# Optimization experiments

Hardware: AMD Instinct MI355X
Metric: run time of the kernel (lower is better)

## Reference

```python
import jax, jax.numpy as jnp
import numpy as np

N_NODES = 50000
N_EDGES = 800000
IN_FEATS = 512
NUM_HEADS = 4
OUT_FEATS = 64
NEG_SLOPE = 0.2


def setup_inputs() -> dict:
    key = jax.random.key(0)
    k1, k2, k3, k4, k5, k6 = jax.random.split(key, 6)
    feat = jax.random.normal(k1, (N_NODES, IN_FEATS), dtype=jnp.float32)
    W = jax.random.normal(k2, (IN_FEATS, NUM_HEADS * OUT_FEATS), dtype=jnp.float32) * (1.0 / np.sqrt(IN_FEATS))
    attn_l = jax.random.normal(k3, (NUM_HEADS, OUT_FEATS), dtype=jnp.float32) * (1.0 / np.sqrt(OUT_FEATS))
    attn_r = jax.random.normal(k4, (NUM_HEADS, OUT_FEATS), dtype=jnp.float32) * (1.0 / np.sqrt(OUT_FEATS))
    src = jax.random.randint(k5, (N_EDGES,), 0, N_NODES, dtype=jnp.int32)
    dst = jax.random.randint(k6, (N_EDGES,), 0, N_NODES, dtype=jnp.int32)
    return {"feat": feat, "W": W, "attn_l": attn_l, "attn_r": attn_r, "src": src, "dst": dst}


def reference(feat, W, attn_l, attn_r, src, dst):
    N = feat.shape[0]
    H, D = attn_l.shape
    # node-wise projection: fc(feat).view(N, H, D)
    ft = (feat @ W).reshape(N, H, D)
    # per-node attention logits
    el = jnp.einsum('nhd,hd->nh', ft, attn_l)  # [N, H]
    er = jnp.einsum('nhd,hd->nh', ft, attn_r)  # [N, H]
    # edge-wise score: leaky_relu(el[u] + er[v])
    e = jax.nn.leaky_relu(el[src] + er[dst], negative_slope=NEG_SLOPE)  # [E, H]
    # segment softmax over incoming edges of each destination node
    e_max = jax.ops.segment_max(e, dst, num_segments=N)  # [N, H]
    e_max = jnp.where(jnp.isfinite(e_max), e_max, 0.0)
    exp_e = jnp.exp(e - e_max[dst])  # [E, H]
    denom = jax.ops.segment_sum(exp_e, dst, num_segments=N)  # [N, H]
    a = exp_e / denom[dst]  # [E, H]
    # weighted message aggregation: sum_u a(u,v) * ft[u]
    msg = ft[src] * a[:, :, None]  # [E, H, D]
    out = jax.ops.segment_sum(msg, dst, num_segments=N)  # [N, H, D]
    return out.reshape(N, H * D)
```

## Files before the change

kernel.cpp:

```cpp
#include <hip/hip_runtime.h>
#include <hip/hip_fp16.h>

#define N_NODES 50000
#define N_EDGES 800000
#define IN_F    512
#define NH      4
#define DH      64
#define HD      256
#define NEG     0.2f
#define MAXDEG  64

typedef __attribute__((ext_vector_type(8))) short bf16x8;
typedef __attribute__((ext_vector_type(4))) float f32x4;

__device__ __forceinline__ unsigned short f2bf(float x) {
    unsigned u = __float_as_uint(x);
    unsigned r = (u + 0x7FFFu + ((u >> 16) & 1u)) >> 16;
    return (unsigned short)r;
}
__device__ __forceinline__ float bf2f(unsigned short b) {
    return __uint_as_float((unsigned)b << 16);
}
__device__ __forceinline__ unsigned short f2h(float x) {
    __half h = __float2half_rn(x);
    return *(unsigned short*)&h;
}
__device__ __forceinline__ float h2f(unsigned short us) {
    __half h = *(__half*)&us;
    return __half2float(h);
}

#define NZB ((N_NODES + 255) / 256)
__global__ __launch_bounds__(256) void setup_kernel(const float* __restrict__ W,
                                                    unsigned short* __restrict__ WtbT,
                                                    int* __restrict__ counts) {
    int b = blockIdx.x;
    if (b < NZB) {
        int i = b * 256 + threadIdx.x;
        if (i < N_NODES) counts[i] = 0;
    } else {
        int i = (b - NZB) * 256 + threadIdx.x;
        if (i < IN_F * HD) {
            int k = i >> 8;
            int n = i & 255;
            int t  = k >> 6;
            int kk = k & 63;
            int g  = kk >> 3;
            int w8 = kk & 7;
            WtbT[(size_t)t * 16384 + g * 2048 + n * 8 + w8] = f2bf(W[i]);
        }
    }
}

#define LDPA 72
__global__ __launch_bounds__(256) void gemm_kernel(const float* __restrict__ A,
                                                   const unsigned short* __restrict__ WtbT,
                                                   const float* __restrict__ attn_l,
                                                   const float* __restrict__ attn_r,
                                                   unsigned short* __restrict__ Cb,
                                                   float* __restrict__ el,
                                                   float* __restrict__ er) {
    __shared__ short A_s[2][64][LDPA];

    const int tid  = threadIdx.x;
    const int lane = tid & 63;
    const int w    = tid >> 6;
    const int lm   = lane & 15;
    const int quad = lane >> 4;
    const int row0 = blockIdx.x * 64;

    const int srow = tid >> 3;
    const int sc8  = (tid & 7) * 8;

    f32x4 acc[4][4] = {};
    float4 pa[4];

#define LOAD_A(KT)                                                             \
    {                                                                          \
        int g0 = row0 + srow; g0 = (g0 < N_NODES) ? g0 : (N_NODES - 1);        \
        const float* ap0 = A + (size_t)g0 * IN_F + (KT) + sc8;                 \
        pa[0] = *(const float4*)ap0; pa[1] = *(const float4*)(ap0 + 4);        \
        int g1 = row0 + 32 + srow; g1 = (g1 < N_NODES) ? g1 : (N_NODES - 1);   \
        const float* ap1 = A + (size_t)g1 * IN_F + (KT) + sc8;                 \
        pa[2] = *(const float4*)ap1; pa[3] = *(const float4*)(ap1 + 4);        \
    }

#define CVT_STORE(BUF)                                                         \
    {                                                                          \
        bf16x8 s;                                                              \
        s[0] = (short)f2bf(pa[0].x); s[1] = (short)f2bf(pa[0].y);              \
        s[2] = (short)f2bf(pa[0].z); s[3] = (short)f2bf(pa[0].w);              \
        s[4] = (short)f2bf(pa[1].x); s[5] = (short)f2bf(pa[1].y);              \
        s[6] = (short)f2bf(pa[1].z); s[7] = (short)f2bf(pa[1].w);              \
        *(bf16x8*)(&A_s[BUF][srow][sc8]) = s;                                  \
        s[0] = (short)f2bf(pa[2].x); s[1] = (short)f2bf(pa[2].y);              \
        s[2] = (short)f2bf(pa[2].z); s[3] = (short)f2bf(pa[2].w);              \
        s[4] = (short)f2bf(pa[3].x); s[5] = (short)f2bf(pa[3].y);              \
        s[6] = (short)f2bf(pa[3].z); s[7] = (short)f2bf(pa[3].w);              \
        *(bf16x8*)(&A_s[BUF][32 + srow][sc8]) = s;                             \
    }

    LOAD_A(0);
    CVT_STORE(0);
    __syncthreads();

    for (int t = 0; t < 8; t++) {
        const int cur = t & 1;
        const unsigned short* bq =
            WtbT + (size_t)t * 16384 + ((quad << 8) + w * 64 + lm) * 8;
        bf16x8 bfr0[4], bfr1[4];
#pragma unroll
        for (int j = 0; j < 4; j++) bfr0[j] = *(const bf16x8*)(bq + j * 128);
#pragma unroll
        for (int j = 0; j < 4; j++) bfr1[j] = *(const bf16x8*)(bq + 8192 + j * 128);

        if (t < 7) LOAD_A((t + 1) * 64);

        {
            bf16x8 af[4];
#pragma unroll
            for (int i = 0; i < 4; i++)
                af[i] = *(const bf16x8*)(&A_s[cur][i * 16 + lm][quad * 8]);
#pragma unroll
            for (int i = 0; i < 4; i++)
#pragma unroll
                for (int j = 0; j < 4; j++)
                    acc[i][j] = __builtin_amdgcn_mfma_f32_16x16x32_bf16(
                        af[i], bfr0[j], acc[i][j], 0, 0, 0);
        }
        {
            bf16x8 af[4];
#pragma unroll
            for (int i = 0; i < 4; i++)
                af[i] = *(const bf16x8*)(&A_s[cur][i * 16 + lm][32 + quad * 8]);
#pragma unroll
            for (int i = 0; i < 4; i++)
#pragma unroll
                for (int j = 0; j < 4; j++)
                    acc[i][j] = __builtin_amdgcn_mfma_f32_16x16x32_bf16(
                        af[i], bfr1[j], acc[i][j], 0, 0, 0);
        }

        if (t < 7) {
            CVT_STORE(cur ^ 1);
            __syncthreads();
        }
    }
#undef LOAD_A
#undef CVT_STORE

#pragma unroll
    for (int i = 0; i < 4; i++) {
#pragma unroll
        for (int j = 0; j < 4; j++) {
            int gcol = w * 64 + j * 16 + lm;
#pragma unroll
            for (int r = 0; r < 4; r++) {
                int grow = row0 + i * 16 + quad * 4 + r;
                if (grow < N_NODES)
                    Cb[(size_t)grow * HD + gcol] = f2bf(acc[i][j][r]);
            }
        }
    }

    {
        float al[4], ar[4];
#pragma unroll
        for (int j = 0; j < 4; j++) {
            al[j] = attn_l[w * DH + j * 16 + lm];
            ar[j] = attn_r[w * DH + j * 16 + lm];
        }
#pragma unroll
        for (int i = 0; i < 4; i++) {
#pragma unroll
            for (int r = 0; r < 4; r++) {
                float sl = 0.f, sr = 0.f;
#pragma unroll
                for (int j = 0; j < 4; j++) {
                    sl += acc[i][j][r] * al[j];
                    sr += acc[i][j][r] * ar[j];
                }
#pragma unroll
                for (int off = 8; off > 0; off >>= 1) {
                    sl += __shfl_xor(sl, off);
                    sr += __shfl_xor(sr, off);
                }
                if (lm == 0) {
                    int grow = row0 + i * 16 + quad * 4 + r;
                    if (grow < N_NODES) {
                        el[(size_t)grow * NH + w] = sl;
                        er[(size_t)grow * NH + w] = sr;
                    }
                }
            }
        }
    }
}

__device__ __forceinline__ float lrelu_exp(float x) {
    float y = fmaxf(x, NEG * x);
    return fminf(__expf(y), 60000.f);
}

__global__ __launch_bounds__(256) void place_kernel(const int* __restrict__ src,
                                                    const int* __restrict__ dst,
                                                    const float* __restrict__ el,
                                                    const float* __restrict__ er,
                                                    int* __restrict__ counts,
                                                    int4* __restrict__ recs) {
    int e = blockIdx.x * blockDim.x + threadIdx.x;
    if (e >= N_EDGES) return;
    int u = src[e], v = dst[e];
    float4 l = *(const float4*)(el + (size_t)u * NH);
    float4 r = *(const float4*)(er + (size_t)v * NH);
    float w0 = lrelu_exp(l.x + r.x);
    float w1 = lrelu_exp(l.y + r.y);
    float w2 = lrelu_exp(l.z + r.z);
    float w3 = lrelu_exp(l.w + r.w);
    int4 rec;
    rec.x = u;
    rec.y = (int)(((unsigned)f2h(w1) << 16) | (unsigned)f2h(w0));
    rec.z = (int)(((unsigned)f2h(w3) << 16) | (unsigned)f2h(w2));
    rec.w = 0;
    int j = atomicAdd(&counts[v], 1);
    if (j < MAXDEG) recs[(size_t)v * MAXDEG + j] = rec;
}

__global__ __launch_bounds__(256) void agg_kernel(const unsigned short* __restrict__ ftb,
                                                  const int4* __restrict__ recs,
                                                  const int* __restrict__ counts,
                                                  float* __restrict__ out) {
    int wv   = (blockIdx.x * blockDim.x + threadIdx.x) >> 6;
    int lane = threadIdx.x & 63;
    if (wv >= N_NODES) return;

    int deg = counts[wv];
    deg = (deg > MAXDEG) ? MAXDEG : deg;
    const int h    = lane >> 4;
    const int sh   = (h & 1) * 16;
    const int wsel = 1 + (h >> 1);
    const size_t foff = (size_t)lane * 4;
    const unsigned* rp = (const unsigned*)(recs + (size_t)wv * MAXDEG);

    float4 acc = make_float4(0.f, 0.f, 0.f, 0.f);
    float dsum = 0.f;

    const int n8 = deg >> 3;
    for (int b = 0; b < n8; b++) {
        const unsigned* q = rp + b * 32;
        unsigned u0 = q[0],  p0 = q[0  + wsel];
        unsigned u1 = q[4],  p1 = q[4  + wsel];
        unsigned u2 = q[8],  p2 = q[8  + wsel];
        unsigned u3 = q[12], p3 = q[12 + wsel];
        unsigned u4 = q[16], p4 = q[16 + wsel];
        unsigned u5 = q[20], p5 = q[20 + wsel];
        unsigned u6 = q[24], p6 = q[24 + wsel];
        unsigned u7 = q[28], p7 = q[28 + wsel];
        ushort4 f0 = *(const ushort4*)(ftb + (size_t)u0 * HD + foff);
        ushort4 f1 = *(const ushort4*)(ftb + (size_t)u1 * HD + foff);
        ushort4 f2 = *(const ushort4*)(ftb + (size_t)u2 * HD + foff);
        ushort4 f3 = *(const ushort4*)(ftb + (size_t)u3 * HD + foff);
        ushort4 f4 = *(const ushort4*)(ftb + (size_t)u4 * HD + foff);
        ushort4 f5 = *(const ushort4*)(ftb + (size_t)u5 * HD + foff);
        ushort4 f6 = *(const ushort4*)(ftb + (size_t)u6 * HD + foff);
        ushort4 f7 = *(const ushort4*)(ftb + (size_t)u7 * HD + foff);
        float w0 = h2f((unsigned short)((p0 >> sh) & 0xFFFFu));
        float w1 = h2f((unsigned short)((p1 >> sh) & 0xFFFFu));
        float w2 = h2f((unsigned short)((p2 >> sh) & 0xFFFFu));
        float w3 = h2f((unsigned short)((p3 >> sh) & 0xFFFFu));
        float w4 = h2f((unsigned short)((p4 >> sh) & 0xFFFFu));
        float w5 = h2f((unsigned short)((p5 >> sh) & 0xFFFFu));
        float w6 = h2f((unsigned short)((p6 >> sh) & 0xFFFFu));
        float w7 = h2f((unsigned short)((p7 >> sh) & 0xFFFFu));
        acc.x += w0 * bf2f(f0.x) + w1 * bf2f(f1.x) + w2 * bf2f(f2.x) + w3 * bf2f(f3.x)
               + w4 * bf2f(f4.x) + w5 * bf2f(f5.x) + w6 * bf2f(f6.x) + w7 * bf2f(f7.x);
        acc.y += w0 * bf2f(f0.y) + w1 * bf2f(f1.y) + w2 * bf2f(f2.y) + w3 * bf2f(f3.y)
               + w4 * bf2f(f4.y) + w5 * bf2f(f5.y) + w6 * bf2f(f6.y) + w7 * bf2f(f7.y);
        acc.z += w0 * bf2f(f0.z) + w1 * bf2f(f1.z) + w2 * bf2f(f2.z) + w3 * bf2f(f3.z)
               + w4 * bf2f(f4.z) + w5 * bf2f(f5.z) + w6 * bf2f(f6.z) + w7 * bf2f(f7.z);
        acc.w += w0 * bf2f(f0.w) + w1 * bf2f(f1.w) + w2 * bf2f(f2.w) + w3 * bf2f(f3.w)
               + w4 * bf2f(f4.w) + w5 * bf2f(f5.w) + w6 * bf2f(f6.w) + w7 * bf2f(f7.w);
        dsum += ((w0 + w1) + (w2 + w3)) + ((w4 + w5) + (w6 + w7));
    }
    {
        const int p0i = n8 * 8;
        const int rem = deg - p0i;
        if (rem > 0) {
            const unsigned* q = rp + p0i * 4;
            unsigned u0 = q[0];
            unsigned u1 = (1 < rem) ? q[4]  : u0;
            unsigned u2 = (2 < rem) ? q[8]  : u0;
            unsigned u3 = (3 < rem) ? q[12] : u0;
            unsigned u4 = (4 < rem) ? q[16] : u0;
            unsigned u5 = (5 < rem) ? q[20] : u0;
            unsigned u6 = (6 < rem) ? q[24] : u0;
            unsigned p0 = q[0 + wsel];
            unsigned p1 = (1 < rem) ? q[4  + wsel] : 0u;
            unsigned p2 = (2 < rem) ? q[8  + wsel] : 0u;
            unsigned p3 = (3 < rem) ? q[12 + wsel] : 0u;
            unsigned p4 = (4 < rem) ? q[16 + wsel] : 0u;
            unsigned p5 = (5 < rem) ? q[20 + wsel] : 0u;
            unsigned p6 = (6 < rem) ? q[24 + wsel] : 0u;
            ushort4 f0 = *(const ushort4*)(ftb + (size_t)u0 * HD + foff);
            ushort4 f1 = *(const ushort4*)(ftb + (size_t)u1 * HD + foff);
            ushort4 f2 = *(const ushort4*)(ftb + (size_t)u2 * HD + foff);
            ushort4 f3 = *(const ushort4*)(ftb + (size_t)u3 * HD + foff);
            ushort4 f4 = *(const ushort4*)(ftb + (size_t)u4 * HD + foff);
            ushort4 f5 = *(const ushort4*)(ftb + (size_t)u5 * HD + foff);
            ushort4 f6 = *(const ushort4*)(ftb + (size_t)u6 * HD + foff);
            float w0 = h2f((unsigned short)((p0 >> sh) & 0xFFFFu));
            float w1 = h2f((unsigned short)((p1 >> sh) & 0xFFFFu));
            float w2 = h2f((unsigned short)((p2 >> sh) & 0xFFFFu));
            float w3 = h2f((unsigned short)((p3 >> sh) & 0xFFFFu));
            float w4 = h2f((unsigned short)((p4 >> sh) & 0xFFFFu));
            float w5 = h2f((unsigned short)((p5 >> sh) & 0xFFFFu));
            float w6 = h2f((unsigned short)((p6 >> sh) & 0xFFFFu));
            acc.x += w0 * bf2f(f0.x) + w1 * bf2f(f1.x) + w2 * bf2f(f2.x) + w3 * bf2f(f3.x)
                   + w4 * bf2f(f4.x) + w5 * bf2f(f5.x) + w6 * bf2f(f6.x);
            acc.y += w0 * bf2f(f0.y) + w1 * bf2f(f1.y) + w2 * bf2f(f2.y) + w3 * bf2f(f3.y)
                   + w4 * bf2f(f4.y) + w5 * bf2f(f5.y) + w6 * bf2f(f6.y);
            acc.z += w0 * bf2f(f0.z) + w1 * bf2f(f1.z) + w2 * bf2f(f2.z) + w3 * bf2f(f3.z)
                   + w4 * bf2f(f4.z) + w5 * bf2f(f5.z) + w6 * bf2f(f6.z);
            acc.w += w0 * bf2f(f0.w) + w1 * bf2f(f1.w) + w2 * bf2f(f2.w) + w3 * bf2f(f3.w)
                   + w4 * bf2f(f4.w) + w5 * bf2f(f5.w) + w6 * bf2f(f6.w);
            dsum += ((w0 + w1) + (w2 + w3)) + ((w4 + w5) + w6);
        }
    }

    float inv = (dsum > 0.f) ? (1.f / dsum) : 0.f;
    acc.x *= inv; acc.y *= inv; acc.z *= inv; acc.w *= inv;
    *(float4*)(out + (size_t)wv * HD + foff) = acc;
}

extern "C" void kernel_launch(void* const* d_in, const int* in_sizes, int n_in,
                              void* d_out, int out_size, void* d_ws, size_t ws_size,
                              hipStream_t stream) {
    const float* feat   = (const float*)d_in[0];
    const float* W      = (const float*)d_in[1];
    const float* attn_l = (const float*)d_in[2];
    const float* attn_r = (const float*)d_in[3];
    const int*   src    = (const int*)d_in[4];
    const int*   dst    = (const int*)d_in[5];
    float* out = (float*)d_out;

    char* p = (char*)d_ws;
    auto alloc = [&](size_t bytes) -> char* {
        char* r = p;
        p += (bytes + 255) & ~(size_t)255;
        return r;
    };
    unsigned short* ftb    = (unsigned short*)alloc((size_t)N_NODES * HD * 2);
    unsigned short* WtbT   = (unsigned short*)alloc((size_t)IN_F * HD * 2);
    float*          el     = (float*)alloc((size_t)N_NODES * NH * 4);
    float*          er     = (float*)alloc((size_t)N_NODES * NH * 4);
    int4*           recs   = (int4*)alloc((size_t)N_NODES * MAXDEG * 16);
    int*            counts = (int*)alloc((size_t)N_NODES * 4);

    setup_kernel<<<NZB + (IN_F * HD + 255) / 256, 256, 0, stream>>>(W, WtbT, counts);
    gemm_kernel<<<(N_NODES + 63) / 64, 256, 0, stream>>>(feat, WtbT, attn_l, attn_r,
                                                         ftb, el, er);
    place_kernel<<<(N_EDGES + 255) / 256, 256, 0, stream>>>(src, dst, el, er,
                                                            counts, recs);
    agg_kernel<<<(N_NODES + 3) / 4, 256, 0, stream>>>(ftb, recs, counts, out);
}
```

Measured before the change: 305.5 us.

## Restructure GEMM so each wave computes a 16-row by full-width tile without LDS

The projection GEMM switches from a 64-row block tile staged through double-buffered shared memory to one where each wave independently owns 16 rows and all 256 output columns. A-fragments are loaded straight from global memory and converted to bf16 in registers, and B chunks are streamed through a three-slot register ring. This removes LDS traffic and block barriers. It also computes all four heads' attention logits per wave and writes them as float4. The cost is that each wave now reloads the full W matrix, with four times less B reuse per load than before, and uses more accumulator registers.

Result: slower. 327.8 us (+7.3%).

```diff
diff --git a/kernel.cpp b/kernel.cpp
--- a/kernel.cpp
+++ b/kernel.cpp
@@ -9,6 +9,7 @@
 #define HD      256
 #define NEG     0.2f
 #define MAXDEG  64
+#define NWAVES  (N_NODES / 16)
 
 typedef __attribute__((ext_vector_type(8))) short bf16x8;
 typedef __attribute__((ext_vector_type(4))) float f32x4;
@@ -52,7 +53,6 @@
     }
 }
 
-#define LDPA 72
 __global__ __launch_bounds__(256) void gemm_kernel(const float* __restrict__ A,
                                                    const unsigned short* __restrict__ WtbT,
                                                    const float* __restrict__ attn_l,
@@ -60,138 +60,112 @@
                                                    unsigned short* __restrict__ Cb,
                                                    float* __restrict__ el,
                                                    float* __restrict__ er) {
-    __shared__ short A_s[2][64][LDPA];
-
     const int tid  = threadIdx.x;
+    const int wv   = (blockIdx.x * 256 + tid) >> 6;
+    if (wv >= NWAVES) return;
     const int lane = tid & 63;
-    const int w    = tid >> 6;
     const int lm   = lane & 15;
     const int quad = lane >> 4;
-    const int row0 = blockIdx.x * 64;
-
-    const int srow = tid >> 3;
-    const int sc8  = (tid & 7) * 8;
-
-    f32x4 acc[4][4] = {};
-    float4 pa[4];
-
-#define LOAD_A(KT)                                                             \
-    {                                                                          \
-        int g0 = row0 + srow; g0 = (g0 < N_NODES) ? g0 : (N_NODES - 1);        \
-        const float* ap0 = A + (size_t)g0 * IN_F + (KT) + sc8;                 \
-        pa[0] = *(const float4*)ap0; pa[1] = *(const float4*)(ap0 + 4);        \
-        int g1 = row0 + 32 + srow; g1 = (g1 < N_NODES) ? g1 : (N_NODES - 1);   \
-        const float* ap1 = A + (size_t)g1 * IN_F + (KT) + sc8;                 \
-        pa[2] = *(const float4*)ap1; pa[3] = *(const float4*)(ap1 + 4);        \
-    }
-
-#define CVT_STORE(BUF)                                                         \
-    {                                                                          \
-        bf16x8 s;                                                              \
-        s[0] = (short)f2bf(pa[0].x); s[1] = (short)f2bf(pa[0].y);              \
-        s[2] = (short)f2bf(pa[0].z); s[3] = (short)f2bf(pa[0].w);              \
-        s[4] = (short)f2bf(pa[1].x); s[5] = (short)f2bf(pa[1].y);              \
-        s[6] = (short)f2bf(pa[1].z); s[7] = (short)f2bf(pa[1].w);              \
-        *(bf16x8*)(&A_s[BUF][srow][sc8]) = s;                                  \
-        s[0] = (short)f2bf(pa[2].x); s[1] = (short)f2bf(pa[2].y);              \
-        s[2] = (short)f2bf(pa[2].z); s[3] = (short)f2bf(pa[2].w);              \
-        s[4] = (short)f2bf(pa[3].x); s[5] = (short)f2bf(pa[3].y);              \
-        s[6] = (short)f2bf(pa[3].z); s[7] = (short)f2bf(pa[3].w);              \
-        *(bf16x8*)(&A_s[BUF][32 + srow][sc8]) = s;                             \
-    }
-
-    LOAD_A(0);
-    CVT_STORE(0);
-    __syncthreads();
+
+    const int row0 = wv * 16;
+    const float* arow = A + (size_t)(row0 + lm) * IN_F + quad * 8;
+    const unsigned short* bbase = WtbT + quad * 2048 + (size_t)lm * 8;
+
+    f32x4 acc[16] = {};
+    float4 pa0, pa1, pa2, pa3;
+    bf16x8 bch[3][4];
+
+    pa0 = *(const float4*)(arow + 0);
+    pa1 = *(const float4*)(arow + 4);
+    pa2 = *(const float4*)(arow + 32);
+    pa3 = *(const float4*)(arow + 36);
 
     for (int t = 0; t < 8; t++) {
-        const int cur = t & 1;
-        const unsigned short* bq =
-            WtbT + (size_t)t * 16384 + ((quad << 8) + w * 64 + lm) * 8;
-        bf16x8 bfr0[4], bfr1[4];
-#pragma unroll
-        for (int j = 0; j < 4; j++) bfr0[j] = *(const bf16x8*)(bq + j * 128);
-#pragma unroll
-        for (int j = 0; j < 4; j++) bfr1[j] = *(const bf16x8*)(bq + 8192 + j * 128);
-
-        if (t < 7) LOAD_A((t + 1) * 64);
-
-        {
-            bf16x8 af[4];
-#pragma unroll
-            for (int i = 0; i < 4; i++)
-                af[i] = *(const bf16x8*)(&A_s[cur][i * 16 + lm][quad * 8]);
-#pragma unroll
-            for (int i = 0; i < 4; i++)
-#pragma unroll
-                for (int j = 0; j < 4; j++)
-                    acc[i][j] = __builtin_amdgcn_mfma_f32_16x16x32_bf16(
-                        af[i], bfr0[j], acc[i][j], 0, 0, 0);
-        }
-        {
-            bf16x8 af[4];
-#pragma unroll
-            for (int i = 0; i < 4; i++)
-                af[i] = *(const bf16x8*)(&A_s[cur][i * 16 + lm][32 + quad * 8]);
-#pragma unroll
-            for (int i = 0; i < 4; i++)
-#pragma unroll
-                for (int j = 0; j < 4; j++)
-                    acc[i][j] = __builtin_amdgcn_mfma_f32_16x16x32_bf16(
-                        af[i], bfr1[j], acc[i][j], 0, 0, 0);
-        }
-
-        if (t < 7) {
-            CVT_STORE(cur ^ 1);
-            __syncthreads();
-        }
-    }
-#undef LOAD_A
-#undef CVT_STORE
-
-#pragma unroll
-    for (int i = 0; i < 4; i++) {
-#pragma unroll
-        for (int j = 0; j < 4; j++) {
-            int gcol = w * 64 + j * 16 + lm;
-#pragma unroll
-            for (int r = 0; r < 4; r++) {
-                int grow = row0 + i * 16 + quad * 4 + r;
-                if (grow < N_NODES)
-                    Cb[(size_t)grow * HD + gcol] = f2bf(acc[i][j][r]);
-            }
+        bf16x8 af0, af1;
+        af0[0] = (short)f2bf(pa0.x); af0[1] = (short)f2bf(pa0.y);
+        af0[2] = (short)f2bf(pa0.z); af0[3] = (short)f2bf(pa0.w);
+        af0[4] = (short)f2bf(pa1.x); af0[5] = (short)f2bf(pa1.y);
+        af0[6] = (short)f2bf(pa1.z); af0[7] = (short)f2bf(pa1.w);
+        af1[0] = (short)f2bf(pa2.x); af1[1] = (short)f2bf(pa2.y);
+        af1[2] = (short)f2bf(pa2.z); af1[3] = (short)f2bf(pa2.w);
+        af1[4] = (short)f2bf(pa3.x); af1[5] = (short)f2bf(pa3.y);
+        af1[6] = (short)f2bf(pa3.z); af1[7] = (short)f2bf(pa3.w);
+
+        const unsigned short* bt = bbase + (size_t)t * 16384;
+#pragma unroll
+        for (int jx = 0; jx < 4; jx++)
+            bch[0][jx] = *(const bf16x8*)(bt + jx * 128);
+#pragma unroll
+        for (int jx = 0; jx < 4; jx++)
+            bch[1][jx] = *(const bf16x8*)(bt + 512 + jx * 128);
+
+#pragma unroll
+        for (int c = 0; c < 8; c++) {
+            if (c < 6) {
+                const int cc  = c + 2;
+                const unsigned short* p = bt + (cc >> 2) * 8192 + (cc & 3) * 512;
+#pragma unroll
+                for (int jx = 0; jx < 4; jx++)
+                    bch[cc % 3][jx] = *(const bf16x8*)(p + jx * 128);
+            }
+            if (c == 6 && t < 7) {
+                const float* an = arow + (t + 1) * 64;
+                pa0 = *(const float4*)an;        pa1 = *(const float4*)(an + 4);
+                pa2 = *(const float4*)(an + 32); pa3 = *(const float4*)(an + 36);
+            }
+#pragma unroll
+            for (int jx = 0; jx < 4; jx++) {
+                if ((c >> 2) == 0)
+                    acc[(c & 3) * 4 + jx] = __builtin_amdgcn_mfma_f32_16x16x32_bf16(
+                        af0, bch[c % 3][jx], acc[(c & 3) * 4 + jx], 0, 0, 0);
+                else
+                    acc[(c & 3) * 4 + jx] = __builtin_amdgcn_mfma_f32_16x16x32_bf16(
+                        af1, bch[c % 3][jx], acc[(c & 3) * 4 + jx], 0, 0, 0);
+            }
+        }
+    }
+
+#pragma unroll
+    for (int j = 0; j < 16; j++) {
+        const int gcol = j * 16 + lm;
+#pragma unroll
+        for (int r = 0; r < 4; r++) {
+            const int grow = row0 + quad * 4 + r;
+            Cb[(size_t)grow * HD + gcol] = f2bf(acc[j][r]);
         }
     }
 
     {
-        float al[4], ar[4];
-#pragma unroll
-        for (int j = 0; j < 4; j++) {
-            al[j] = attn_l[w * DH + j * 16 + lm];
-            ar[j] = attn_r[w * DH + j * 16 + lm];
-        }
-#pragma unroll
-        for (int i = 0; i < 4; i++) {
-#pragma unroll
-            for (int r = 0; r < 4; r++) {
-                float sl = 0.f, sr = 0.f;
-#pragma unroll
-                for (int j = 0; j < 4; j++) {
-                    sl += acc[i][j][r] * al[j];
-                    sr += acc[i][j][r] * ar[j];
+        float al[16], ar[16];
+#pragma unroll
+        for (int j = 0; j < 16; j++) {
+            al[j] = attn_l[j * 16 + lm];
+            ar[j] = attn_r[j * 16 + lm];
+        }
+#pragma unroll
+        for (int r = 0; r < 4; r++) {
+            float sl[4], sr[4];
+#pragma unroll
+            for (int h = 0; h < 4; h++) {
+                float a = 0.f, b = 0.f;
+#pragma unroll
+                for (int jj = 0; jj < 4; jj++) {
+                    a += acc[h * 4 + jj][r] * al[h * 4 + jj];
+                    b += acc[h * 4 + jj][r] * ar[h * 4 + jj];
                 }
 #pragma unroll
                 for (int off = 8; off > 0; off >>= 1) {
-                    sl += __shfl_xor(sl, off);
-                    sr += __shfl_xor(sr, off);
+                    a += __shfl_xor(a, off);
+                    b += __shfl_xor(b, off);
                 }
-                if (lm == 0) {
-                    int grow = row0 + i * 16 + quad * 4 + r;
-                    if (grow < N_NODES) {
-                        el[(size_t)grow * NH + w] = sl;
-                        er[(size_t)grow * NH + w] = sr;
-                    }
-                }
+                sl[h] = a; sr[h] = b;
+            }
+            if (lm == 0) {
+                const int grow = row0 + quad * 4 + r;
+                *(float4*)(el + (size_t)grow * NH) =
+                    make_float4(sl[0], sl[1], sl[2], sl[3]);
+                *(float4*)(er + (size_t)grow * NH) =
+                    make_float4(sr[0], sr[1], sr[2], sr[3]);
             }
         }
     }
@@ -357,8 +331,8 @@
     int*            counts = (int*)alloc((size_t)N_NODES * 4);
 
     setup_kernel<<<NZB + (IN_F * HD + 255) / 256, 256, 0, stream>>>(W, WtbT, counts);
-    gemm_kernel<<<(N_NODES + 63) / 64, 256, 0, stream>>>(feat, WtbT, attn_l, attn_r,
-                                                         ftb, el, er);
+    gemm_kernel<<<(NWAVES + 3) / 4, 256, 0, stream>>>(feat, WtbT, attn_l, attn_r,
+                                                      ftb, el, er);
     place_kernel<<<(N_EDGES + 255) / 256, 256, 0, stream>>>(src, dst, el, er,
                                                             counts, recs);
     agg_kernel<<<(N_NODES + 3) / 4, 256, 0, stream>>>(ftb, recs, counts, out);
```

## Split GEMM columns across grid and stage B through swizzled LDS via direct loads

Applied to the files above, without the earlier changes.

The projection GEMM now uses a 2D grid, with each block computing a 64x128 column half (two heads) instead of the full 256 columns. The bf16 weight tiles are laid out with an XOR swizzle and copied into LDS with global_load_lds, replacing per-wave global reads of B fragments. A-loads are prefetched two stages ahead, and barriers use explicit waitcnt. This gives more blocks and less register pressure (acc shrinks from 16 to 8 tiles), at the cost of reading the fp32 feature matrix twice and using more LDS per block.

New measurement: 308.2 us. About the same (+0.9%).

```diff
diff --git a/kernel.cpp b/kernel.cpp
--- a/kernel.cpp
+++ b/kernel.cpp
@@ -47,7 +47,10 @@
             int kk = k & 63;
             int g  = kk >> 3;
             int w8 = kk & 7;
-            WtbT[(size_t)t * 16384 + g * 2048 + n * 8 + w8] = f2bf(W[i]);
+            int cb = n >> 7;
+            int nl = n & 127;
+            WtbT[((size_t)t * 2 + cb) * 8192 + (nl * 8 + (g ^ (nl & 7))) * 8 + w8]
+                = f2bf(W[i]);
         }
     }
 }
@@ -61,6 +64,7 @@
                                                    float* __restrict__ el,
                                                    float* __restrict__ er) {
     __shared__ short A_s[2][64][LDPA];
+    __shared__ short B_s[2][8192];
 
     const int tid  = threadIdx.x;
     const int lane = tid & 63;
@@ -68,95 +72,110 @@
     const int lm   = lane & 15;
     const int quad = lane >> 4;
     const int row0 = blockIdx.x * 64;
+    const int cb   = blockIdx.y;
 
     const int srow = tid >> 3;
     const int sc8  = (tid & 7) * 8;
 
-    f32x4 acc[4][4] = {};
-    float4 pa[4];
-
-#define LOAD_A(KT)                                                             \
+    f32x4  acc[2][4] = {};
+    float4 pa[2][4];
+
+#define LOAD_A(KT, P)                                                          \
     {                                                                          \
         int g0 = row0 + srow; g0 = (g0 < N_NODES) ? g0 : (N_NODES - 1);        \
         const float* ap0 = A + (size_t)g0 * IN_F + (KT) + sc8;                 \
-        pa[0] = *(const float4*)ap0; pa[1] = *(const float4*)(ap0 + 4);        \
+        pa[P][0] = *(const float4*)ap0; pa[P][1] = *(const float4*)(ap0 + 4);  \
         int g1 = row0 + 32 + srow; g1 = (g1 < N_NODES) ? g1 : (N_NODES - 1);   \
         const float* ap1 = A + (size_t)g1 * IN_F + (KT) + sc8;                 \
-        pa[2] = *(const float4*)ap1; pa[3] = *(const float4*)(ap1 + 4);        \
-    }
-
-#define CVT_STORE(BUF)                                                         \
+        pa[P][2] = *(const float4*)ap1; pa[P][3] = *(const float4*)(ap1 + 4);  \
+    }
+
+#define STAGE_B(T, BUF)                                                         \
+    {                                                                           \
+        const char* gsrc = (const char*)(WtbT + ((size_t)(T) * 2 + cb) * 8192)  \
+                           + tid * 16;                                          \
+        char* ldst = (char*)&B_s[BUF][0] + tid * 16;                            \
+        _Pragma("unroll")                                                       \
+        for (int s = 0; s < 4; s++)                                             \
+            __builtin_amdgcn_global_load_lds(                                   \
+                (const __attribute__((address_space(1))) unsigned int*)(gsrc + s * 4096), \
+                (__attribute__((address_space(3))) unsigned int*)(ldst + s * 4096),       \
+                16, 0, 0);                                                      \
+    }
+
+#define CVT_STORE(P, BUF)                                                      \
     {                                                                          \
         bf16x8 s;                                                              \
-        s[0] = (short)f2bf(pa[0].x); s[1] = (short)f2bf(pa[0].y);              \
-        s[2] = (short)f2bf(pa[0].z); s[3] = (short)f2bf(pa[0].w);              \
-        s[4] = (short)f2bf(pa[1].x); s[5] = (short)f2bf(pa[1].y);              \
-        s[6] = (short)f2bf(pa[1].z); s[7] = (short)f2bf(pa[1].w);              \
+        s[0] = (short)f2bf(pa[P][0].x); s[1] = (short)f2bf(pa[P][0].y);        \
+        s[2] = (short)f2bf(pa[P][0].z); s[3] = (short)f2bf(pa[P][0].w);        \
+        s[4] = (short)f2bf(pa[P][1].x); s[5] = (short)f2bf(pa[P][1].y);        \
+        s[6] = (short)f2bf(pa[P][1].z); s[7] = (short)f2bf(pa[P][1].w);        \
         *(bf16x8*)(&A_s[BUF][srow][sc8]) = s;                                  \
-        s[0] = (short)f2bf(pa[2].x); s[1] = (short)f2bf(pa[2].y);              \
-        s[2] = (short)f2bf(pa[2].z); s[3] = (short)f2bf(pa[2].w);              \
-        s[4] = (short)f2bf(pa[3].x); s[5] = (short)f2bf(pa[3].y);              \
-        s[6] = (short)f2bf(pa[3].z); s[7] = (short)f2bf(pa[3].w);              \
+        s[0] = (short)f2bf(pa[P][2].x); s[1] = (short)f2bf(pa[P][2].y);        \
+        s[2] = (short)f2bf(pa[P][2].z); s[3] = (short)f2bf(pa[P][2].w);        \
+        s[4] = (short)f2bf(pa[P][3].x); s[5] = (short)f2bf(pa[P][3].y);        \
+        s[6] = (short)f2bf(pa[P][3].z); s[7] = (short)f2bf(pa[P][3].w);        \
         *(bf16x8*)(&A_s[BUF][32 + srow][sc8]) = s;                             \
     }
 
-    LOAD_A(0);
-    CVT_STORE(0);
-    __syncthreads();
-
+    LOAD_A(0, 0);
+    STAGE_B(0, 0);
+    CVT_STORE(0, 0);
+    LOAD_A(64, 1);
+    asm volatile("s_waitcnt vmcnt(4) lgkmcnt(0)" ::: "memory");
+    __builtin_amdgcn_s_barrier();
+    __builtin_amdgcn_sched_barrier(0);
+
+#pragma unroll
     for (int t = 0; t < 8; t++) {
         const int cur = t & 1;
-        const unsigned short* bq =
-            WtbT + (size_t)t * 16384 + ((quad << 8) + w * 64 + lm) * 8;
-        bf16x8 bfr0[4], bfr1[4];
-#pragma unroll
-        for (int j = 0; j < 4; j++) bfr0[j] = *(const bf16x8*)(bq + j * 128);
-#pragma unroll
-        for (int j = 0; j < 4; j++) bfr1[j] = *(const bf16x8*)(bq + 8192 + j * 128);
-
-        if (t < 7) LOAD_A((t + 1) * 64);
-
-        {
-            bf16x8 af[4];
-#pragma unroll
-            for (int i = 0; i < 4; i++)
-                af[i] = *(const bf16x8*)(&A_s[cur][i * 16 + lm][quad * 8]);
-#pragma unroll
-            for (int i = 0; i < 4; i++)
+        if (t < 7) STAGE_B(t + 1, cur ^ 1);
+        if (t < 6) LOAD_A((t + 2) * 64, t & 1);
+
+#pragma unroll
+        for (int kk2 = 0; kk2 < 2; kk2++) {
+            bf16x8 af[2], bfr[4];
+#pragma unroll
+            for (int i = 0; i < 2; i++)
+                af[i] = *(const bf16x8*)(
+                    &A_s[cur][(w >> 1) * 32 + i * 16 + lm][kk2 * 32 + quad * 8]);
+#pragma unroll
+            for (int j = 0; j < 4; j++) {
+                int nl = (w & 1) * 64 + j * 16 + lm;
+                int g  = kk2 * 4 + quad;
+                int p  = nl * 8 + (g ^ (lm & 7));
+                bfr[j] = *(const bf16x8*)(&B_s[cur][p * 8]);
+            }
+#pragma unroll
+            for (int i = 0; i < 2; i++)
 #pragma unroll
                 for (int j = 0; j < 4; j++)
                     acc[i][j] = __builtin_amdgcn_mfma_f32_16x16x32_bf16(
-                        af[i], bfr0[j], acc[i][j], 0, 0, 0);
-        }
-        {
-            bf16x8 af[4];
-#pragma unroll
-            for (int i = 0; i < 4; i++)
-                af[i] = *(const bf16x8*)(&A_s[cur][i * 16 + lm][32 + quad * 8]);
-#pragma unroll
-            for (int i = 0; i < 4; i++)
-#pragma unroll
-                for (int j = 0; j < 4; j++)
-                    acc[i][j] = __builtin_amdgcn_mfma_f32_16x16x32_bf16(
-                        af[i], bfr1[j], acc[i][j], 0, 0, 0);
+                        af[i], bfr[j], acc[i][j], 0, 0, 0);
         }
 
         if (t < 7) {
-            CVT_STORE(cur ^ 1);
-            __syncthreads();
+            CVT_STORE((t + 1) & 1, cur ^ 1);
+            if (t < 6)
+                asm volatile("s_waitcnt vmcnt(4) lgkmcnt(0)" ::: "memory");
+            else
+                asm volatile("s_waitcnt vmcnt(0) lgkmcnt(0)" ::: "memory");
+            __builtin_amdgcn_s_barrier();
+            __builtin_amdgcn_sched_barrier(0);
         }
     }
 #undef LOAD_A
+#undef STAGE_B
 #undef CVT_STORE
 
 #pragma unroll
-    for (int i = 0; i < 4; i++) {
+    for (int i = 0; i < 2; i++) {
 #pragma unroll
         for (int j = 0; j < 4; j++) {
-            int gcol = w * 64 + j * 16 + lm;
+            int gcol = cb * 128 + (w & 1) * 64 + j * 16 + lm;
 #pragma unroll
             for (int r = 0; r < 4; r++) {
-                int grow = row0 + i * 16 + quad * 4 + r;
+                int grow = row0 + (w >> 1) * 32 + i * 16 + quad * 4 + r;
                 if (grow < N_NODES)
                     Cb[(size_t)grow * HD + gcol] = f2bf(acc[i][j][r]);
             }
@@ -164,14 +183,15 @@
     }
 
     {
+        const int h = cb * 2 + (w & 1);
         float al[4], ar[4];
 #pragma unroll
         for (int j = 0; j < 4; j++) {
-            al[j] = attn_l[w * DH + j * 16 + lm];
-            ar[j] = attn_r[w * DH + j * 16 + lm];
-        }
-#pragma unroll
-        for (int i = 0; i < 4; i++) {
+            al[j] = attn_l[h * DH + j * 16 + lm];
+            ar[j] = attn_r[h * DH + j * 16 + lm];
+        }
+#pragma unroll
+        for (int i = 0; i < 2; i++) {
 #pragma unroll
             for (int r = 0; r < 4; r++) {
                 float sl = 0.f, sr = 0.f;
@@ -186,10 +206,10 @@
                     sr += __shfl_xor(sr, off);
                 }
                 if (lm == 0) {
-                    int grow = row0 + i * 16 + quad * 4 + r;
+                    int grow = row0 + (w >> 1) * 32 + i * 16 + quad * 4 + r;
                     if (grow < N_NODES) {
-                        el[(size_t)grow * NH + w] = sl;
-                        er[(size_t)grow * NH + w] = sr;
+                        el[(size_t)grow * NH + h] = sl;
+                        er[(size_t)grow * NH + h] = sr;
                     }
                 }
             }
@@ -357,8 +377,10 @@
     int*            counts = (int*)alloc((size_t)N_NODES * 4);
 
     setup_kernel<<<NZB + (IN_F * HD + 255) / 256, 256, 0, stream>>>(W, WtbT, counts);
-    gemm_kernel<<<(N_NODES + 63) / 64, 256, 0, stream>>>(feat, WtbT, attn_l, attn_r,
-                                                         ftb, el, er);
+    {
+        dim3 g((N_NODES + 63) / 64, 2);
+        gemm_kernel<<<g, 256, 0, stream>>>(feat, WtbT, attn_l, attn_r, ftb, el, er);
+    }
     place_kernel<<<(N_EDGES + 255) / 256, 256, 0, stream>>>(src, dst, el, er,
                                                             counts, recs);
     agg_kernel<<<(N_NODES + 3) / 4, 256, 0, stream>>>(ftb, recs, counts, out);
```
